# Kernel tuning notes

Hardware: AMD Instinct MI355X
Metric: run time of the kernel (lower is better)

Reference implementation:

```python
import jax, jax.numpy as jnp
import numpy as np

DIM = 1024
HEADS = 8
DIM_HEAD = 64
HIDDEN = HEADS * DIM_HEAD  # 512
SCALE = DIM_HEAD ** -0.5
BATCH = 16384
EPS = 1e-12  # F.normalize eps


def setup_inputs() -> dict:
    key = jax.random.key(0)
    k0, k1, k2 = jax.random.split(key, 3)
    x = jax.random.normal(k0, (BATCH, DIM), dtype=jnp.float32)
    w_qkv = jax.random.normal(k1, (3 * HIDDEN, DIM), dtype=jnp.float32) * 0.02
    w_out = jax.random.normal(k2, (DIM, HIDDEN), dtype=jnp.float32) * 0.02
    b_out = jnp.zeros((DIM,), dtype=jnp.float32)
    g = jnp.ones((1, DIM), dtype=jnp.float32)
    return {"x": x, "w_qkv": w_qkv, "w_out": w_out, "b_out": b_out, "g": g}


def reference(x, w_qkv, w_out, b_out, g):
    b = x.shape[0]
    # Conv1d(kernel=1, no bias) on n=1 sequence == matmul with (3*hidden, dim) weight
    qkv = x @ w_qkv.T  # (b, 3*hidden)
    q, k, v = jnp.split(qkv, 3, axis=1)  # each (b, hidden)
    # rearrange 'b (h c) n -> b h c n' with n=1 -> (b, h, c)
    q = q.reshape(b, HEADS, DIM_HEAD)
    k = k.reshape(b, HEADS, DIM_HEAD)
    v = v.reshape(b, HEADS, DIM_HEAD)
    # q.softmax(dim=-2) is over the c axis
    q = jax.nn.softmax(q, axis=-1) * SCALE
    # k.softmax(dim=-1) is over the n axis of size 1 -> all ones (kept faithful)
    k = jax.nn.softmax(k[..., None], axis=-1)[..., 0]
    # context = einsum('bhdn,bhen->bhde', k, v); out = einsum('bhde,bhdn->bhen', context, q)
    # with n=1 this collapses to out_e = (sum_d k_d q_d) * v_e; fused to avoid (b,h,d,e)
    s = jnp.einsum('bhd,bhd->bh', k, q)  # (b, h)
    out = s[..., None] * v  # (b, h, e)
    out = out.reshape(b, HIDDEN)  # 'b h c n -> b (h c) n', squeeze(-1)
    # Linear(hidden, dim)
    out = out @ w_out.T + b_out  # (b, dim)
    # RMSNorm_MLP: F.normalize(x, dim=1) * g * sqrt(dim)
    norm = jnp.linalg.norm(out, axis=1, keepdims=True)
    out = out / jnp.maximum(norm, EPS) * g * jnp.sqrt(jnp.float32(DIM))
    return out
```

## Files before the change

### kernel.cpp

```cpp
#include <hip/hip_runtime.h>
#include <hip/hip_bf16.h>


typedef __attribute__((ext_vector_type(8))) short bf16x8;
typedef __attribute__((ext_vector_type(4))) float f32x4;

struct alignas(16) bfvec8 { __hip_bfloat16 h[8]; };

__device__ __forceinline__ bfvec8 pack8(float4 a, float4 b) {
    bfvec8 o;
    o.h[0] = __float2bfloat16(a.x); o.h[1] = __float2bfloat16(a.y);
    o.h[2] = __float2bfloat16(a.z); o.h[3] = __float2bfloat16(a.w);
    o.h[4] = __float2bfloat16(b.x); o.h[5] = __float2bfloat16(b.y);
    o.h[6] = __float2bfloat16(b.z); o.h[7] = __float2bfloat16(b.w);
    return o;
}

__global__ __launch_bounds__(256)
void weff_fused(const float* __restrict__ Wo, const float* __restrict__ Wv,
                __hip_bfloat16* __restrict__ Weff) {
    __shared__ __align__(16) __hip_bfloat16 As[64 * 32];
    __shared__ __align__(16) __hip_bfloat16 Bs[64 * 32];
    __shared__ __align__(16) float Bf[32 * 65];

    const int tid  = threadIdx.x;
    const int lane = tid & 63;
    const int wave = tid >> 6;
    const int wm   = wave >> 1;
    const int wn   = wave & 1;
    const int quad = lane >> 4;
    const int tr   = lane & 15;
    const int m0   = blockIdx.y * 64;
    const int n0   = blockIdx.x * 64;

    f32x4 acc[2][2];
#pragma unroll
    for (int i = 0; i < 2; ++i)
#pragma unroll
        for (int j = 0; j < 2; ++j)
            acc[i][j] = (f32x4){0.f, 0.f, 0.f, 0.f};

    for (int kt = 0; kt < 512; kt += 32) {
        {
            int r = tid >> 2, c = tid & 3;
            int s = (r >> 1) & 3;
            int kg = (c ^ s) << 3;
            const float* sp = Wo + (size_t)(m0 + r) * 512 + kt + kg;
            float4 a = *(const float4*)sp, b = *(const float4*)(sp + 4);
            *(bfvec8*)(As + r * 32 + (c << 3)) = pack8(a, b);
        }
        {
            int kr = tid >> 3, c8 = (tid & 7) << 3;
            const float* sp = Wv + (size_t)(kt + kr) * 1024 + n0 + c8;
            float4 a = *(const float4*)sp, b = *(const float4*)(sp + 4);
            *(float4*)(Bf + kr * 65 + c8)     = a;
            *(float4*)(Bf + kr * 65 + c8 + 4) = b;
        }
        __syncthreads();
        {
            int n = tid >> 2, cc = tid & 3, k8 = cc << 3;
            float4 a, b;
            a.x = Bf[(k8 + 0) * 65 + n]; a.y = Bf[(k8 + 1) * 65 + n];
            a.z = Bf[(k8 + 2) * 65 + n]; a.w = Bf[(k8 + 3) * 65 + n];
            b.x = Bf[(k8 + 4) * 65 + n]; b.y = Bf[(k8 + 5) * 65 + n];
            b.z = Bf[(k8 + 6) * 65 + n]; b.w = Bf[(k8 + 7) * 65 + n];
            int cs = cc ^ ((n >> 1) & 3);
            *(bfvec8*)(Bs + n * 32 + cs * 8) = pack8(a, b);
        }
        __syncthreads();

        bf16x8 af[2], bf[2];
#pragma unroll
        for (int mi = 0; mi < 2; ++mi) {
            int r = wm * 32 + mi * 16 + tr;
            int c = quad ^ ((r >> 1) & 3);
            af[mi] = *(const bf16x8*)(As + r * 32 + c * 8);
        }
#pragma unroll
        for (int ni = 0; ni < 2; ++ni) {
            int r = wn * 32 + ni * 16 + tr;
            int c = quad ^ ((r >> 1) & 3);
            bf[ni] = *(const bf16x8*)(Bs + r * 32 + c * 8);
        }
#pragma unroll
        for (int mi = 0; mi < 2; ++mi)
#pragma unroll
            for (int ni = 0; ni < 2; ++ni)
                acc[mi][ni] = __builtin_amdgcn_mfma_f32_16x16x32_bf16(
                    af[mi], bf[ni], acc[mi][ni], 0, 0, 0);
        __syncthreads();
    }

#pragma unroll
    for (int mi = 0; mi < 2; ++mi)
#pragma unroll
        for (int ni = 0; ni < 2; ++ni) {
            const int col = n0 + wn * 32 + ni * 16 + tr;
#pragma unroll
            for (int r = 0; r < 4; ++r) {
                const int row = m0 + wm * 32 + mi * 16 + quad * 4 + r;
                Weff[(size_t)row * 1024 + col] =
                    __float2bfloat16(acc[mi][ni][r] * 0.125f);
            }
        }
}

__global__ __launch_bounds__(256)
void main_gemm(const float* __restrict__ X,
               const __hip_bfloat16* __restrict__ Bt,
               const float* __restrict__ bias,
               __hip_bfloat16* __restrict__ Y) {
    __shared__ __align__(16) __hip_bfloat16 As[128 * 64];
    __shared__ __align__(16) __hip_bfloat16 Bs[128 * 64];

    const int tid  = threadIdx.x;
    const int lane = tid & 63;
    const int wave = tid >> 6;
    const int wm   = wave >> 1;
    const int wn   = wave & 1;
    const int quad = lane >> 4;
    const int tr   = lane & 15;

    const int b   = blockIdx.x;
    const int xcd = b & 7;
    const int t   = b >> 3;
    const int nt  = t & 7;
    const int mt  = (t >> 3) * 8 + xcd;
    const int m0  = mt * 128;
    const int n0  = nt * 128;

    int rr[4], kgg[4];
    size_t abase[4];
#pragma unroll
    for (int i = 0; i < 4; ++i) {
        int L = i * 256 + tid;
        rr[i]  = L >> 3;
        int c  = L & 7;
        kgg[i] = (c ^ (rr[i] & 7)) << 3;
        abase[i] = (size_t)(m0 + rr[i]) * 1024 + kgg[i];
    }

    f32x4 acc[4][4];
#pragma unroll
    for (int i = 0; i < 4; ++i)
#pragma unroll
        for (int j = 0; j < 4; ++j)
            acc[i][j] = (f32x4){0.f, 0.f, 0.f, 0.f};

    float4 pa[4], pb[4];
#pragma unroll
    for (int i = 0; i < 4; ++i) {
        const float* s = X + abase[i];
        pa[i] = *(const float4*)s;
        pb[i] = *(const float4*)(s + 4);
    }

    for (int kt = 0; kt < 1024; kt += 64) {
#pragma unroll
        for (int i = 0; i < 4; ++i) {
            int L = i * 256 + tid;
            const __hip_bfloat16* gb = Bt + (size_t)(n0 + rr[i]) * 1024 + kt + kgg[i];
            __builtin_amdgcn_global_load_lds(
                (const __attribute__((address_space(1))) void*)gb,
                (__attribute__((address_space(3))) void*)(Bs + (size_t)L * 8), 16, 0, 0);
        }
#pragma unroll
        for (int i = 0; i < 4; ++i) {
            int L = i * 256 + tid;
            *(bfvec8*)(As + (size_t)L * 8) = pack8(pa[i], pb[i]);
        }
        __syncthreads();

        if (kt + 64 < 1024) {
#pragma unroll
            for (int i = 0; i < 4; ++i) {
                const float* s = X + abase[i] + kt + 64;
                pa[i] = *(const float4*)s;
                pb[i] = *(const float4*)(s + 4);
            }
        }

#pragma unroll
        for (int ko = 0; ko < 2; ++ko) {
            bf16x8 af[4], bf[4];
#pragma unroll
            for (int mi = 0; mi < 4; ++mi) {
                int r = wm * 64 + mi * 16 + tr;
                int c = (ko * 4 + quad) ^ (r & 7);
                af[mi] = *(const bf16x8*)(As + (r * 8 + c) * 8);
            }
#pragma unroll
            for (int ni = 0; ni < 4; ++ni) {
                int r = wn * 64 + ni * 16 + tr;
                int c = (ko * 4 + quad) ^ (r & 7);
                bf[ni] = *(const bf16x8*)(Bs + (r * 8 + c) * 8);
            }
#pragma unroll
            for (int mi = 0; mi < 4; ++mi)
#pragma unroll
                for (int ni = 0; ni < 4; ++ni)
                    acc[mi][ni] = __builtin_amdgcn_mfma_f32_16x16x32_bf16(
                        af[mi], bf[ni], acc[mi][ni], 0, 0, 0);
        }
        __syncthreads();
    }

#pragma unroll
    for (int mi = 0; mi < 4; ++mi)
#pragma unroll
        for (int ni = 0; ni < 4; ++ni) {
            const int col = n0 + wn * 64 + ni * 16 + tr;
            const float bv = bias[col];
#pragma unroll
            for (int r = 0; r < 4; ++r) {
                const int row = m0 + wm * 64 + mi * 16 + quad * 4 + r;
                Y[(size_t)row * 1024 + col] = __float2bfloat16(acc[mi][ni][r] + bv);
            }
        }
}

__global__ __launch_bounds__(256)
void rmsnorm2(const __hip_bfloat16* __restrict__ y, const float* __restrict__ g,
              float* __restrict__ out) {
    const int wave = threadIdx.x >> 6;
    const int sub  = wave >> 1;
    const int t    = threadIdx.x & 127;
    const int row  = blockIdx.x * 2 + sub;
    const size_t base = (size_t)row * 1024 + t * 8;

    union { uint4 u; ushort s[8]; } U;
    U.u = *(const uint4*)(y + base);
    float v[8];
#pragma unroll
    for (int j = 0; j < 8; ++j)
        v[j] = __bfloat162float(*(const __hip_bfloat16*)&U.s[j]);

    float ss = 0.f;
#pragma unroll
    for (int j = 0; j < 8; ++j) ss += v[j] * v[j];
#pragma unroll
    for (int off = 32; off > 0; off >>= 1)
        ss += __shfl_down(ss, off, 64);

    __shared__ float wsum[4];
    if ((threadIdx.x & 63) == 0) wsum[wave] = ss;
    __syncthreads();
    const float total = wsum[sub * 2] + wsum[sub * 2 + 1];
    const float sc = 32.0f / fmaxf(sqrtf(total), 1e-12f);

    const float4 g0 = *(const float4*)(g + t * 8);
    const float4 g1 = *(const float4*)(g + t * 8 + 4);
    float4 o0, o1;
    o0.x = v[0] * sc * g0.x; o0.y = v[1] * sc * g0.y;
    o0.z = v[2] * sc * g0.z; o0.w = v[3] * sc * g0.w;
    o1.x = v[4] * sc * g1.x; o1.y = v[5] * sc * g1.y;
    o1.z = v[6] * sc * g1.z; o1.w = v[7] * sc * g1.w;
    *(float4*)(out + base)     = o0;
    *(float4*)(out + base + 4) = o1;
}

extern "C" void kernel_launch(void* const* d_in, const int* in_sizes, int n_in,
                              void* d_out, int out_size, void* d_ws, size_t ws_size,
                              hipStream_t stream) {
    const float* x     = (const float*)d_in[0];
    const float* w_qkv = (const float*)d_in[1];
    const float* w_out = (const float*)d_in[2];
    const float* b_out = (const float*)d_in[3];
    const float* g     = (const float*)d_in[4];

    const int B = 16384, D = 1024, H = 512;
    const float* wv = w_qkv + (size_t)2 * H * D;

    char* ws = (char*)d_ws;
    size_t off = 0;
    __hip_bfloat16* weff_bf = (__hip_bfloat16*)(ws + off); off += (size_t)D * D * 2;
    __hip_bfloat16* y_bf    = (__hip_bfloat16*)(ws + off); off += (size_t)B * D * 2;

    weff_fused<<<dim3(D / 64, D / 64), 256, 0, stream>>>(w_out, wv, weff_bf);
    main_gemm<<<1024, 256, 0, stream>>>(x, weff_bf, b_out, y_bf);
    rmsnorm2<<<B / 2, 256, 0, stream>>>(y_bf, g, (float*)d_out);
}
```

Before: 190.5 us.

## Double-buffer LDS tiles in main GEMM to overlap loads with MFMA

Doubles the shared-memory buffers for A and B in the main GEMM and restructures the k-loop so the next tile's global-to-LDS B load and the A bf16 conversion/store happen while MFMAs run on the current tile. This cuts the loop from two barriers per iteration to one, with manual s_waitcnt and sched_barrier control. It doubles LDS use to 64KB per block, which may lower occupancy, and relies on hand-counted vmcnt values being correct.

```diff
diff --git a/kernel.cpp b/kernel.cpp
--- a/kernel.cpp
+++ b/kernel.cpp
@@ -105,13 +105,42 @@
         }
 }
 
+
+__device__ __forceinline__ void mfma_tile(const __hip_bfloat16* Ac,
+                                          const __hip_bfloat16* Bc,
+                                          f32x4 (&acc)[4][4],
+                                          int wm, int wn, int quad, int tr) {
+#pragma unroll
+    for (int ko = 0; ko < 2; ++ko) {
+        bf16x8 af[4], bf[4];
+#pragma unroll
+        for (int mi = 0; mi < 4; ++mi) {
+            int r = wm * 64 + mi * 16 + tr;
+            int c = (ko * 4 + quad) ^ (r & 7);
+            af[mi] = *(const bf16x8*)(Ac + (r * 8 + c) * 8);
+        }
+#pragma unroll
+        for (int ni = 0; ni < 4; ++ni) {
+            int r = wn * 64 + ni * 16 + tr;
+            int c = (ko * 4 + quad) ^ (r & 7);
+            bf[ni] = *(const bf16x8*)(Bc + (r * 8 + c) * 8);
+        }
+#pragma unroll
+        for (int mi = 0; mi < 4; ++mi)
+#pragma unroll
+            for (int ni = 0; ni < 4; ++ni)
+                acc[mi][ni] = __builtin_amdgcn_mfma_f32_16x16x32_bf16(
+                    af[mi], bf[ni], acc[mi][ni], 0, 0, 0);
+    }
+}
+
 __global__ __launch_bounds__(256)
 void main_gemm(const float* __restrict__ X,
                const __hip_bfloat16* __restrict__ Bt,
                const float* __restrict__ bias,
                __hip_bfloat16* __restrict__ Y) {
-    __shared__ __align__(16) __hip_bfloat16 As[128 * 64];
-    __shared__ __align__(16) __hip_bfloat16 Bs[128 * 64];
+    __shared__ __align__(16) __hip_bfloat16 As[2 * 128 * 64];
+    __shared__ __align__(16) __hip_bfloat16 Bs[2 * 128 * 64];
 
     const int tid  = threadIdx.x;
     const int lane = tid & 63;
@@ -123,21 +152,24 @@
 
     const int b   = blockIdx.x;
     const int xcd = b & 7;
-    const int t   = b >> 3;
-    const int nt  = t & 7;
-    const int mt  = (t >> 3) * 8 + xcd;
-    const int m0  = mt * 128;
-    const int n0  = nt * 128;
-
-    int rr[4], kgg[4];
+    const int tb  = b >> 3;
+    const int ntl = tb & 7;
+    const int mtl = (tb >> 3) * 8 + xcd;
+    const int m0  = mtl * 128;
+    const int n0  = ntl * 128;
+
+    int rr[4], kgg[4], ldst[4];
     size_t abase[4];
+    const __hip_bfloat16* bbase[4];
 #pragma unroll
     for (int i = 0; i < 4; ++i) {
         int L = i * 256 + tid;
-        rr[i]  = L >> 3;
-        int c  = L & 7;
-        kgg[i] = (c ^ (rr[i] & 7)) << 3;
+        rr[i]   = L >> 3;
+        int c   = L & 7;
+        kgg[i]  = (c ^ (rr[i] & 7)) << 3;
+        ldst[i] = L * 8;
         abase[i] = (size_t)(m0 + rr[i]) * 1024 + kgg[i];
+        bbase[i] = Bt + (size_t)(n0 + rr[i]) * 1024 + kgg[i];
     }
 
     f32x4 acc[4][4];
@@ -146,6 +178,11 @@
 #pragma unroll
         for (int j = 0; j < 4; ++j)
             acc[i][j] = (f32x4){0.f, 0.f, 0.f, 0.f};
+
+    __hip_bfloat16* Ac = As;
+    __hip_bfloat16* An = As + 128 * 64;
+    __hip_bfloat16* Bc = Bs;
+    __hip_bfloat16* Bn = Bs + 128 * 64;
 
     float4 pa[4], pb[4];
 #pragma unroll
@@ -154,56 +191,56 @@
         pa[i] = *(const float4*)s;
         pb[i] = *(const float4*)(s + 4);
     }
-
-    for (int kt = 0; kt < 1024; kt += 64) {
-#pragma unroll
-        for (int i = 0; i < 4; ++i) {
-            int L = i * 256 + tid;
-            const __hip_bfloat16* gb = Bt + (size_t)(n0 + rr[i]) * 1024 + kt + kgg[i];
+#pragma unroll
+    for (int i = 0; i < 4; ++i)
+        __builtin_amdgcn_global_load_lds(
+            (const __attribute__((address_space(1))) void*)(bbase[i]),
+            (__attribute__((address_space(3))) void*)(Bc + ldst[i]), 16, 0, 0);
+#pragma unroll
+    for (int i = 0; i < 4; ++i)
+        *(bfvec8*)(Ac + ldst[i]) = pack8(pa[i], pb[i]);
+    __syncthreads();
+#pragma unroll
+    for (int i = 0; i < 4; ++i) {
+        const float* s = X + abase[i] + 64;
+        pa[i] = *(const float4*)s;
+        pb[i] = *(const float4*)(s + 4);
+    }
+
+    for (int t = 0; t < 15; ++t) {
+        const int koff = (t + 1) * 64;
+
+#pragma unroll
+        for (int i = 0; i < 4; ++i)
             __builtin_amdgcn_global_load_lds(
-                (const __attribute__((address_space(1))) void*)gb,
-                (__attribute__((address_space(3))) void*)(Bs + (size_t)L * 8), 16, 0, 0);
-        }
-#pragma unroll
-        for (int i = 0; i < 4; ++i) {
-            int L = i * 256 + tid;
-            *(bfvec8*)(As + (size_t)L * 8) = pack8(pa[i], pb[i]);
-        }
-        __syncthreads();
-
-        if (kt + 64 < 1024) {
+                (const __attribute__((address_space(1))) void*)(bbase[i] + koff),
+                (__attribute__((address_space(3))) void*)(Bn + ldst[i]), 16, 0, 0);
+        __builtin_amdgcn_sched_barrier(0);
+
+        mfma_tile(Ac, Bc, acc, wm, wn, quad, tr);
+
+#pragma unroll
+        for (int i = 0; i < 4; ++i)
+            *(bfvec8*)(An + ldst[i]) = pack8(pa[i], pb[i]);
+
+        if (t < 14) {
 #pragma unroll
             for (int i = 0; i < 4; ++i) {
-                const float* s = X + abase[i] + kt + 64;
+                const float* s = X + abase[i] + koff + 64;
                 pa[i] = *(const float4*)s;
                 pb[i] = *(const float4*)(s + 4);
             }
-        }
-
-#pragma unroll
-        for (int ko = 0; ko < 2; ++ko) {
-            bf16x8 af[4], bf[4];
-#pragma unroll
-            for (int mi = 0; mi < 4; ++mi) {
-                int r = wm * 64 + mi * 16 + tr;
-                int c = (ko * 4 + quad) ^ (r & 7);
-                af[mi] = *(const bf16x8*)(As + (r * 8 + c) * 8);
-            }
-#pragma unroll
-            for (int ni = 0; ni < 4; ++ni) {
-                int r = wn * 64 + ni * 16 + tr;
-                int c = (ko * 4 + quad) ^ (r & 7);
-                bf[ni] = *(const bf16x8*)(Bs + (r * 8 + c) * 8);
-            }
-#pragma unroll
-            for (int mi = 0; mi < 4; ++mi)
-#pragma unroll
-                for (int ni = 0; ni < 4; ++ni)
-                    acc[mi][ni] = __builtin_amdgcn_mfma_f32_16x16x32_bf16(
-                        af[mi], bf[ni], acc[mi][ni], 0, 0, 0);
-        }
-        __syncthreads();
-    }
+            asm volatile("s_waitcnt vmcnt(8) lgkmcnt(0)" ::: "memory");
+        } else {
+            asm volatile("s_waitcnt vmcnt(0) lgkmcnt(0)" ::: "memory");
+        }
+        __builtin_amdgcn_sched_barrier(0);
+        __builtin_amdgcn_s_barrier();
+
+        __hip_bfloat16* tA = Ac; Ac = An; An = tA;
+        __hip_bfloat16* tB = Bc; Bc = Bn; Bn = tB;
+    }
+    mfma_tile(Ac, Bc, acc, wm, wn, quad, tr);
 
 #pragma unroll
     for (int mi = 0; mi < 4; ++mi)
```

Result: no change. 193.4 us (+1.5%).

## Pre-convert X to bf16 in prep kernel and rewrite main GEMM pipeline

Applied to the files above, without the earlier changes.

Adds a grid-stride pass to the Weff prep kernel that converts X to bf16 in a new workspace buffer. The main GEMM can then stream both operands straight into LDS with global_load_lds. The GEMM becomes 256x256 tiles with 512 threads, double-buffered LDS, staged async loads interleaved with MFMA phases, explicit waitcnt/barrier scheduling and setprio. This aims to hide load latency and raise MFMA utilization, at the cost of an extra 32MB bf16 write and read of X and a fragile hand-tuned sync schedule.

```diff
diff --git a/kernel.cpp b/kernel.cpp
--- a/kernel.cpp
+++ b/kernel.cpp
@@ -17,21 +17,34 @@
 }
 
 __global__ __launch_bounds__(256)
-void weff_fused(const float* __restrict__ Wo, const float* __restrict__ Wv,
-                __hip_bfloat16* __restrict__ Weff) {
+void prep(const float* __restrict__ Wo, const float* __restrict__ Wv,
+          __hip_bfloat16* __restrict__ Weff,
+          const float* __restrict__ X, __hip_bfloat16* __restrict__ Xbf) {
     __shared__ __align__(16) __hip_bfloat16 As[64 * 32];
     __shared__ __align__(16) __hip_bfloat16 Bs[64 * 32];
     __shared__ __align__(16) float Bf[32 * 65];
 
-    const int tid  = threadIdx.x;
+    const int tid = threadIdx.x;
+
+    if (blockIdx.x >= 256) {
+        const size_t nv = (size_t)16384 * 1024 / 8;
+        const size_t stride = (size_t)2048 * 256;
+        for (size_t i = (size_t)(blockIdx.x - 256) * 256 + tid; i < nv; i += stride) {
+            const float4 a = *(const float4*)(X + i * 8);
+            const float4 b = *(const float4*)(X + i * 8 + 4);
+            *(bfvec8*)(Xbf + i * 8) = pack8(a, b);
+        }
+        return;
+    }
+
     const int lane = tid & 63;
     const int wave = tid >> 6;
     const int wm   = wave >> 1;
     const int wn   = wave & 1;
     const int quad = lane >> 4;
     const int tr   = lane & 15;
-    const int m0   = blockIdx.y * 64;
-    const int n0   = blockIdx.x * 64;
+    const int m0   = (blockIdx.x >> 4) * 64;
+    const int n0   = (blockIdx.x & 15) * 64;
 
     f32x4 acc[2][2];
 #pragma unroll
@@ -69,7 +82,7 @@
         }
         __syncthreads();
 
-        bf16x8 af[2], bf[2];
+        bf16x8 af[2], bfr[2];
 #pragma unroll
         for (int mi = 0; mi < 2; ++mi) {
             int r = wm * 32 + mi * 16 + tr;
@@ -80,14 +93,14 @@
         for (int ni = 0; ni < 2; ++ni) {
             int r = wn * 32 + ni * 16 + tr;
             int c = quad ^ ((r >> 1) & 3);
-            bf[ni] = *(const bf16x8*)(Bs + r * 32 + c * 8);
+            bfr[ni] = *(const bf16x8*)(Bs + r * 32 + c * 8);
         }
 #pragma unroll
         for (int mi = 0; mi < 2; ++mi)
 #pragma unroll
             for (int ni = 0; ni < 2; ++ni)
                 acc[mi][ni] = __builtin_amdgcn_mfma_f32_16x16x32_bf16(
-                    af[mi], bf[ni], acc[mi][ni], 0, 0, 0);
+                    af[mi], bfr[ni], acc[mi][ni], 0, 0, 0);
         __syncthreads();
     }
 
@@ -105,118 +118,142 @@
         }
 }
 
-__global__ __launch_bounds__(256)
-void main_gemm(const float* __restrict__ X,
+
+#define GLL(gp, lp) __builtin_amdgcn_global_load_lds( \
+    (const __attribute__((address_space(1))) void*)(gp), \
+    (__attribute__((address_space(3))) void*)(lp), 16, 0, 0)
+
+#define STAGE_A(BUF, H, U) do { \
+    GLL(Xbf + Ab0 + (size_t)(H) * 131072 + (size_t)(U) * 64, \
+        sm + (BUF) * 32768 + (H) * 8192 + ldsA);             \
+    GLL(Xbf + Ab1 + (size_t)(H) * 131072 + (size_t)(U) * 64, \
+        sm + (BUF) * 32768 + (H) * 8192 + 4096 + ldsA);      \
+} while (0)
+
+#define STAGE_B(BUF, H, U) do { \
+    GLL(Bt + Bb0 + (size_t)(H) * 131072 + (size_t)(U) * 64,  \
+        sm + (BUF) * 32768 + 16384 + (H) * 8192 + ldsA);     \
+    GLL(Bt + Bb1 + (size_t)(H) * 131072 + (size_t)(U) * 64,  \
+        sm + (BUF) * 32768 + 16384 + (H) * 8192 + 4096 + ldsA); \
+} while (0)
+
+__global__ __launch_bounds__(512, 2)
+void main_gemm(const __hip_bfloat16* __restrict__ Xbf,
                const __hip_bfloat16* __restrict__ Bt,
                const float* __restrict__ bias,
                __hip_bfloat16* __restrict__ Y) {
-    __shared__ __align__(16) __hip_bfloat16 As[128 * 64];
-    __shared__ __align__(16) __hip_bfloat16 Bs[128 * 64];
+    __shared__ __align__(16) __hip_bfloat16 sm[2 * 32768];
 
     const int tid  = threadIdx.x;
     const int lane = tid & 63;
-    const int wave = tid >> 6;
-    const int wm   = wave >> 1;
-    const int wn   = wave & 1;
+    const int wc   = tid >> 6;
     const int quad = lane >> 4;
     const int tr   = lane & 15;
-
-    const int b   = blockIdx.x;
-    const int xcd = b & 7;
-    const int t   = b >> 3;
-    const int nt  = t & 7;
-    const int mt  = (t >> 3) * 8 + xcd;
-    const int m0  = mt * 128;
-    const int n0  = nt * 128;
-
-    int rr[4], kgg[4];
-    size_t abase[4];
-#pragma unroll
-    for (int i = 0; i < 4; ++i) {
-        int L = i * 256 + tid;
-        rr[i]  = L >> 3;
-        int c  = L & 7;
-        kgg[i] = (c ^ (rr[i] & 7)) << 3;
-        abase[i] = (size_t)(m0 + rr[i]) * 1024 + kgg[i];
+    const int rlow = tr & 7;
+
+    const int xcd  = blockIdx.x & 7;
+    const int orig = xcd * 32 + (blockIdx.x >> 3);
+    const int m0   = (orig >> 2) * 256;
+    const int n0   = (orig & 3) * 256;
+
+    const int r0 = tid >> 3,            c0 = tid & 7;
+    const int r1 = (tid + 512) >> 3,    c1 = tid & 7;
+    const size_t Ab0 = (size_t)(m0 + r0) * 1024 + ((c0 ^ (r0 & 7)) << 3);
+    const size_t Ab1 = (size_t)(m0 + r1) * 1024 + ((c1 ^ (r1 & 7)) << 3);
+    const size_t Bb0 = (size_t)(n0 + r0) * 1024 + ((c0 ^ (r0 & 7)) << 3);
+    const size_t Bb1 = (size_t)(n0 + r1) * 1024 + ((c1 ^ (r1 & 7)) << 3);
+    const int ldsA = tid * 8;
+
+    int ac[2];
+#pragma unroll
+    for (int ko = 0; ko < 2; ++ko) ac[ko] = ((ko * 4 + quad) ^ rlow) * 8;
+    const int rdA = tr * 64;
+    const int rdB = wc * 2048 + tr * 64;
+
+    f32x4 acc[16][2];
+#pragma unroll
+    for (int f = 0; f < 16; ++f)
+#pragma unroll
+        for (int ni = 0; ni < 2; ++ni)
+            acc[f][ni] = (f32x4){0.f, 0.f, 0.f, 0.f};
+
+    STAGE_B(0, 0, 0); STAGE_B(0, 1, 0); STAGE_A(0, 0, 0); STAGE_A(0, 1, 0);
+    STAGE_B(1, 0, 1); STAGE_B(1, 1, 1); STAGE_A(1, 0, 1);
+    asm volatile("s_waitcnt vmcnt(6)" ::: "memory");
+    __builtin_amdgcn_s_barrier();
+
+    bf16x8 bfr[2][2];
+
+    for (int it = 0; it < 8; ++it) {
+#pragma unroll
+        for (int rb = 0; rb < 2; ++rb) {
+            const int u = it * 2 + rb;
+#pragma unroll
+            for (int p = 0; p < 4; ++p) {
+                bf16x8 af[4][2];
+#pragma unroll
+                for (int mi = 0; mi < 4; ++mi)
+#pragma unroll
+                    for (int ko = 0; ko < 2; ++ko)
+                        af[mi][ko] = *(const bf16x8*)(
+                            sm + rb * 32768 + p * 4096 + mi * 1024 + rdA + ac[ko]);
+                if (p == 0) {
+#pragma unroll
+                    for (int ni = 0; ni < 2; ++ni)
+#pragma unroll
+                        for (int ko = 0; ko < 2; ++ko)
+                            bfr[ni][ko] = *(const bf16x8*)(
+                                sm + rb * 32768 + 16384 + rdB + ni * 1024 + ac[ko]);
+                }
+
+                if (p == 0)      { if (u + 1 < 16) STAGE_A(rb ^ 1, 1, u + 1); }
+                else if (p == 1) { if (u + 2 < 16) STAGE_B(rb, 0, u + 2); }
+                else if (p == 2) { if (u + 2 < 16) STAGE_B(rb, 1, u + 2); }
+                else             { if (u + 2 < 16) STAGE_A(rb, 0, u + 2); }
+
+                if (p == 0) asm volatile("s_waitcnt lgkmcnt(8)" ::: "memory");
+                __builtin_amdgcn_s_barrier();
+                asm volatile("s_waitcnt lgkmcnt(0)" ::: "memory");
+                __builtin_amdgcn_sched_barrier(0);
+
+                __builtin_amdgcn_s_setprio(1);
+#pragma unroll
+                for (int mi = 0; mi < 4; ++mi)
+#pragma unroll
+                    for (int ni = 0; ni < 2; ++ni)
+#pragma unroll
+                        for (int ko = 0; ko < 2; ++ko)
+                            acc[p * 4 + mi][ni] = __builtin_amdgcn_mfma_f32_16x16x32_bf16(
+                                af[mi][ko], bfr[ni][ko], acc[p * 4 + mi][ni], 0, 0, 0);
+                __builtin_amdgcn_s_setprio(0);
+
+                if (p == 3) {
+                    if (u <= 13)      asm volatile("s_waitcnt vmcnt(6)" ::: "memory");
+                    else if (u == 14) asm volatile("s_waitcnt vmcnt(0)" ::: "memory");
+                    if (u < 15) __builtin_amdgcn_s_barrier();
+                } else {
+                    __builtin_amdgcn_s_barrier();
+                }
+            }
+        }
     }
 
-    f32x4 acc[4][4];
-#pragma unroll
-    for (int i = 0; i < 4; ++i)
-#pragma unroll
-        for (int j = 0; j < 4; ++j)
-            acc[i][j] = (f32x4){0.f, 0.f, 0.f, 0.f};
-
-    float4 pa[4], pb[4];
-#pragma unroll
-    for (int i = 0; i < 4; ++i) {
-        const float* s = X + abase[i];
-        pa[i] = *(const float4*)s;
-        pb[i] = *(const float4*)(s + 4);
+    float bv[2]; int col[2];
+#pragma unroll
+    for (int ni = 0; ni < 2; ++ni) {
+        col[ni] = n0 + wc * 32 + ni * 16 + tr;
+        bv[ni]  = bias[col[ni]];
     }
-
-    for (int kt = 0; kt < 1024; kt += 64) {
-#pragma unroll
-        for (int i = 0; i < 4; ++i) {
-            int L = i * 256 + tid;
-            const __hip_bfloat16* gb = Bt + (size_t)(n0 + rr[i]) * 1024 + kt + kgg[i];
-            __builtin_amdgcn_global_load_lds(
-                (const __attribute__((address_space(1))) void*)gb,
-                (__attribute__((address_space(3))) void*)(Bs + (size_t)L * 8), 16, 0, 0);
-        }
-#pragma unroll
-        for (int i = 0; i < 4; ++i) {
-            int L = i * 256 + tid;
-            *(bfvec8*)(As + (size_t)L * 8) = pack8(pa[i], pb[i]);
-        }
-        __syncthreads();
-
-        if (kt + 64 < 1024) {
-#pragma unroll
-            for (int i = 0; i < 4; ++i) {
-                const float* s = X + abase[i] + kt + 64;
-                pa[i] = *(const float4*)s;
-                pb[i] = *(const float4*)(s + 4);
+#pragma unroll
+    for (int f = 0; f < 16; ++f)
+#pragma unroll
+        for (int ni = 0; ni < 2; ++ni)
+#pragma unroll
+            for (int rr = 0; rr < 4; ++rr) {
+                const int row = m0 + f * 16 + quad * 4 + rr;
+                Y[(size_t)row * 1024 + col[ni]] =
+                    __float2bfloat16(acc[f][ni][rr] + bv[ni]);
             }
-        }
-
-#pragma unroll
-        for (int ko = 0; ko < 2; ++ko) {
-            bf16x8 af[4], bf[4];
-#pragma unroll
-            for (int mi = 0; mi < 4; ++mi) {
-                int r = wm * 64 + mi * 16 + tr;
-                int c = (ko * 4 + quad) ^ (r & 7);
-                af[mi] = *(const bf16x8*)(As + (r * 8 + c) * 8);
-            }
-#pragma unroll
-            for (int ni = 0; ni < 4; ++ni) {
-                int r = wn * 64 + ni * 16 + tr;
-                int c = (ko * 4 + quad) ^ (r & 7);
-                bf[ni] = *(const bf16x8*)(Bs + (r * 8 + c) * 8);
-            }
-#pragma unroll
-            for (int mi = 0; mi < 4; ++mi)
-#pragma unroll
-                for (int ni = 0; ni < 4; ++ni)
-                    acc[mi][ni] = __builtin_amdgcn_mfma_f32_16x16x32_bf16(
-                        af[mi], bf[ni], acc[mi][ni], 0, 0, 0);
-        }
-        __syncthreads();
-    }
-
-#pragma unroll
-    for (int mi = 0; mi < 4; ++mi)
-#pragma unroll
-        for (int ni = 0; ni < 4; ++ni) {
-            const int col = n0 + wn * 64 + ni * 16 + tr;
-            const float bv = bias[col];
-#pragma unroll
-            for (int r = 0; r < 4; ++r) {
-                const int row = m0 + wm * 64 + mi * 16 + quad * 4 + r;
-                Y[(size_t)row * 1024 + col] = __float2bfloat16(acc[mi][ni][r] + bv);
-            }
-        }
 }
 
 __global__ __launch_bounds__(256)
@@ -275,8 +312,9 @@
     size_t off = 0;
     __hip_bfloat16* weff_bf = (__hip_bfloat16*)(ws + off); off += (size_t)D * D * 2;
     __hip_bfloat16* y_bf    = (__hip_bfloat16*)(ws + off); off += (size_t)B * D * 2;
-
-    weff_fused<<<dim3(D / 64, D / 64), 256, 0, stream>>>(w_out, wv, weff_bf);
-    main_gemm<<<1024, 256, 0, stream>>>(x, weff_bf, b_out, y_bf);
+    __hip_bfloat16* x_bf    = (__hip_bfloat16*)(ws + off); off += (size_t)B * D * 2;
+
+    prep<<<256 + 2048, 256, 0, stream>>>(w_out, wv, weff_bf, x, x_bf);
+    main_gemm<<<256, 512, 0, stream>>>(x_bf, weff_bf, b_out, y_bf);
     rmsnorm2<<<B / 2, 256, 0, stream>>>(y_bf, g, (float*)d_out);
 }
```

Measured after the change: 178.4 us. -6.3%, faster.

## Fuse main GEMM with RMSNorm using full-row 64x1024 block tiles

Applied to the files above, without the earlier changes.

Replaces the separate main GEMM and RMSNorm kernels with one kernel. Each 512-thread block computes a full 64-row by 1024-column output tile, so the row norm can be reduced in-block and fp32 output written directly. This removes the bf16 intermediate Y write and re-read and one kernel launch. The main loop double-buffers 32-wide K tiles through LDS using direct global-to-LDS loads, with explicit waitcnt and priority hints. In exchange it uses a large LDS footprint and a single block per CU across 256 blocks, which lowers occupancy and latency hiding.

```diff
diff --git a/kernel.cpp b/kernel.cpp
--- a/kernel.cpp
+++ b/kernel.cpp
@@ -6,6 +6,7 @@
 typedef __attribute__((ext_vector_type(4))) float f32x4;
 
 struct alignas(16) bfvec8 { __hip_bfloat16 h[8]; };
+struct alignas(8)  bfvec4 { __hip_bfloat16 h[4]; };
 
 __device__ __forceinline__ bfvec8 pack8(float4 a, float4 b) {
     bfvec8 o;
@@ -16,9 +17,16 @@
     return o;
 }
 
+__device__ __forceinline__ bfvec4 pack4(float4 a) {
+    bfvec4 o;
+    o.h[0] = __float2bfloat16(a.x); o.h[1] = __float2bfloat16(a.y);
+    o.h[2] = __float2bfloat16(a.z); o.h[3] = __float2bfloat16(a.w);
+    return o;
+}
+
 __global__ __launch_bounds__(256)
-void weff_fused(const float* __restrict__ Wo, const float* __restrict__ Wv,
-                __hip_bfloat16* __restrict__ Weff) {
+void weff_only(const float* __restrict__ Wo, const float* __restrict__ Wv,
+               __hip_bfloat16* __restrict__ Weff) {
     __shared__ __align__(16) __hip_bfloat16 As[64 * 32];
     __shared__ __align__(16) __hip_bfloat16 Bs[64 * 32];
     __shared__ __align__(16) float Bf[32 * 65];
@@ -30,8 +38,8 @@
     const int wn   = wave & 1;
     const int quad = lane >> 4;
     const int tr   = lane & 15;
-    const int m0   = blockIdx.y * 64;
-    const int n0   = blockIdx.x * 64;
+    const int m0   = (blockIdx.x >> 4) * 64;
+    const int n0   = (blockIdx.x & 15) * 64;
 
     f32x4 acc[2][2];
 #pragma unroll
@@ -69,7 +77,7 @@
         }
         __syncthreads();
 
-        bf16x8 af[2], bf[2];
+        bf16x8 af[2], bfr[2];
 #pragma unroll
         for (int mi = 0; mi < 2; ++mi) {
             int r = wm * 32 + mi * 16 + tr;
@@ -80,14 +88,14 @@
         for (int ni = 0; ni < 2; ++ni) {
             int r = wn * 32 + ni * 16 + tr;
             int c = quad ^ ((r >> 1) & 3);
-            bf[ni] = *(const bf16x8*)(Bs + r * 32 + c * 8);
+            bfr[ni] = *(const bf16x8*)(Bs + r * 32 + c * 8);
         }
 #pragma unroll
         for (int mi = 0; mi < 2; ++mi)
 #pragma unroll
             for (int ni = 0; ni < 2; ++ni)
                 acc[mi][ni] = __builtin_amdgcn_mfma_f32_16x16x32_bf16(
-                    af[mi], bf[ni], acc[mi][ni], 0, 0, 0);
+                    af[mi], bfr[ni], acc[mi][ni], 0, 0, 0);
         __syncthreads();
     }
 
@@ -105,158 +113,155 @@
         }
 }
 
-__global__ __launch_bounds__(256)
-void main_gemm(const float* __restrict__ X,
-               const __hip_bfloat16* __restrict__ Bt,
-               const float* __restrict__ bias,
-               __hip_bfloat16* __restrict__ Y) {
-    __shared__ __align__(16) __hip_bfloat16 As[128 * 64];
-    __shared__ __align__(16) __hip_bfloat16 Bs[128 * 64];
+
+#define GLL(gp, lp) __builtin_amdgcn_global_load_lds( \
+    (const __attribute__((address_space(1))) void*)(gp), \
+    (__attribute__((address_space(3))) void*)(lp), 16, 0, 0)
+
+__global__ __launch_bounds__(512, 2)
+void main_fused(const float* __restrict__ X,
+                const __hip_bfloat16* __restrict__ W,
+                const float* __restrict__ bias,
+                const float* __restrict__ g,
+                float* __restrict__ out) {
+    __shared__ __align__(16) __hip_bfloat16 sm[69632];
+    __shared__ float wpart[8][64];
+    __shared__ float scrow[64];
 
     const int tid  = threadIdx.x;
     const int lane = tid & 63;
-    const int wave = tid >> 6;
-    const int wm   = wave >> 1;
-    const int wn   = wave & 1;
+    const int wc   = tid >> 6;
     const int quad = lane >> 4;
     const int tr   = lane & 15;
 
-    const int b   = blockIdx.x;
-    const int xcd = b & 7;
-    const int t   = b >> 3;
-    const int nt  = t & 7;
-    const int mt  = (t >> 3) * 8 + xcd;
-    const int m0  = mt * 128;
-    const int n0  = nt * 128;
-
-    int rr[4], kgg[4];
-    size_t abase[4];
-#pragma unroll
-    for (int i = 0; i < 4; ++i) {
-        int L = i * 256 + tid;
-        rr[i]  = L >> 3;
-        int c  = L & 7;
-        kgg[i] = (c ^ (rr[i] & 7)) << 3;
-        abase[i] = (size_t)(m0 + rr[i]) * 1024 + kgg[i];
-    }
-
-    f32x4 acc[4][4];
-#pragma unroll
-    for (int i = 0; i < 4; ++i)
-#pragma unroll
-        for (int j = 0; j < 4; ++j)
-            acc[i][j] = (f32x4){0.f, 0.f, 0.f, 0.f};
-
-    float4 pa[4], pb[4];
-#pragma unroll
-    for (int i = 0; i < 4; ++i) {
-        const float* s = X + abase[i];
-        pa[i] = *(const float4*)s;
-        pb[i] = *(const float4*)(s + 4);
-    }
-
-    for (int kt = 0; kt < 1024; kt += 64) {
-#pragma unroll
-        for (int i = 0; i < 4; ++i) {
-            int L = i * 256 + tid;
-            const __hip_bfloat16* gb = Bt + (size_t)(n0 + rr[i]) * 1024 + kt + kgg[i];
-            __builtin_amdgcn_global_load_lds(
-                (const __attribute__((address_space(1))) void*)gb,
-                (__attribute__((address_space(3))) void*)(Bs + (size_t)L * 8), 16, 0, 0);
-        }
-#pragma unroll
-        for (int i = 0; i < 4; ++i) {
-            int L = i * 256 + tid;
-            *(bfvec8*)(As + (size_t)L * 8) = pack8(pa[i], pb[i]);
-        }
-        __syncthreads();
-
-        if (kt + 64 < 1024) {
-#pragma unroll
-            for (int i = 0; i < 4; ++i) {
-                const float* s = X + abase[i] + kt + 64;
-                pa[i] = *(const float4*)s;
-                pb[i] = *(const float4*)(s + 4);
+    const int m0 = blockIdx.x * 64;
+
+    const int ra = tid >> 3, q = tid & 7;
+    const int aq = (((q >> 1) ^ (ra & 3)) << 3) + (q & 1) * 4;
+    const float* Ag = X + (size_t)(m0 + ra) * 1024 + aq;
+    const int AdsW = tid * 4;
+
+    const int brow = tid >> 2;
+    const int kswz = (((tid & 3) ^ (brow & 3)) << 3);
+
+    const int ac = ((quad ^ (tr & 3)) << 3);
+
+    f32x4 acc[4][8];
+#pragma unroll
+    for (int mi = 0; mi < 4; ++mi)
+#pragma unroll
+        for (int ni = 0; ni < 8; ++ni)
+            acc[mi][ni] = (f32x4){0.f, 0.f, 0.f, 0.f};
+
+    {
+#pragma unroll
+        for (int i = 0; i < 4; ++i)
+            GLL(W + (size_t)(i * 128 + brow) * 1024 + kswz,
+                sm + 4096 + (i * 512 + tid) * 8);
+        float4 pav = *(const float4*)Ag;
+#pragma unroll
+        for (int i = 4; i < 8; ++i)
+            GLL(W + (size_t)(i * 128 + brow) * 1024 + kswz,
+                sm + 4096 + (i * 512 + tid) * 8);
+        asm volatile("s_waitcnt vmcnt(4)" ::: "memory");
+        *(bfvec4*)(sm + AdsW) = pack4(pav);
+        asm volatile("s_waitcnt vmcnt(0) lgkmcnt(0)" ::: "memory");
+        __builtin_amdgcn_s_barrier();
+    }
+
+#define TILE(U, RB) do { \
+    const int u_ = (U); \
+    float4 pav; \
+    if (u_ < 31) { \
+        const int kt_ = (u_ + 1) * 32; \
+        _Pragma("unroll") \
+        for (int i = 0; i < 4; ++i) \
+            GLL(W + (size_t)(i * 128 + brow) * 1024 + kt_ + kswz, \
+                sm + 4096 + ((RB) ^ 1) * 32768 + (i * 512 + tid) * 8); \
+        pav = *(const float4*)(Ag + kt_); \
+        _Pragma("unroll") \
+        for (int i = 4; i < 8; ++i) \
+            GLL(W + (size_t)(i * 128 + brow) * 1024 + kt_ + kswz, \
+                sm + 4096 + ((RB) ^ 1) * 32768 + (i * 512 + tid) * 8); \
+    } \
+    bf16x8 af[4], bfr[8]; \
+    _Pragma("unroll") \
+    for (int mi = 0; mi < 4; ++mi) \
+        af[mi] = *(const bf16x8*)(sm + (RB) * 2048 + (mi * 16 + tr) * 32 + ac); \
+    _Pragma("unroll") \
+    for (int ni = 0; ni < 8; ++ni) \
+        bfr[ni] = *(const bf16x8*)(sm + 4096 + (RB) * 32768 + \
+                                   (wc * 128 + ni * 16 + tr) * 32 + ac); \
+    asm volatile("s_waitcnt lgkmcnt(0)" ::: "memory"); \
+    __builtin_amdgcn_sched_barrier(0); \
+    __builtin_amdgcn_s_setprio(1); \
+    _Pragma("unroll") \
+    for (int mi = 0; mi < 4; ++mi) \
+        _Pragma("unroll") \
+        for (int ni = 0; ni < 8; ++ni) \
+            acc[mi][ni] = __builtin_amdgcn_mfma_f32_16x16x32_bf16( \
+                af[mi], bfr[ni], acc[mi][ni], 0, 0, 0); \
+    __builtin_amdgcn_s_setprio(0); \
+    if (u_ < 31) { \
+        asm volatile("s_waitcnt vmcnt(4)" ::: "memory"); \
+        *(bfvec4*)(sm + ((RB) ^ 1) * 2048 + AdsW) = pack4(pav); \
+    } \
+    asm volatile("s_waitcnt vmcnt(0) lgkmcnt(0)" ::: "memory"); \
+    __builtin_amdgcn_s_barrier(); \
+} while (0)
+
+    for (int it = 0; it < 16; ++it) {
+        TILE(it * 2,     0);
+        TILE(it * 2 + 1, 1);
+    }
+#undef TILE
+
+    float bvv[8], gvv[8];
+    int coln[8];
+#pragma unroll
+    for (int ni = 0; ni < 8; ++ni) {
+        coln[ni] = wc * 128 + ni * 16 + tr;
+        bvv[ni] = bias[coln[ni]];
+        gvv[ni] = g[coln[ni]];
+    }
+
+#pragma unroll
+    for (int mi = 0; mi < 4; ++mi)
+#pragma unroll
+        for (int rr = 0; rr < 4; ++rr) {
+            float p = 0.f;
+#pragma unroll
+            for (int ni = 0; ni < 8; ++ni) {
+                const float t = acc[mi][ni][rr] + bvv[ni];
+                acc[mi][ni][rr] = t;
+                p += t * t;
             }
-        }
-
-#pragma unroll
-        for (int ko = 0; ko < 2; ++ko) {
-            bf16x8 af[4], bf[4];
-#pragma unroll
-            for (int mi = 0; mi < 4; ++mi) {
-                int r = wm * 64 + mi * 16 + tr;
-                int c = (ko * 4 + quad) ^ (r & 7);
-                af[mi] = *(const bf16x8*)(As + (r * 8 + c) * 8);
-            }
-#pragma unroll
-            for (int ni = 0; ni < 4; ++ni) {
-                int r = wn * 64 + ni * 16 + tr;
-                int c = (ko * 4 + quad) ^ (r & 7);
-                bf[ni] = *(const bf16x8*)(Bs + (r * 8 + c) * 8);
-            }
-#pragma unroll
-            for (int mi = 0; mi < 4; ++mi)
-#pragma unroll
-                for (int ni = 0; ni < 4; ++ni)
-                    acc[mi][ni] = __builtin_amdgcn_mfma_f32_16x16x32_bf16(
-                        af[mi], bf[ni], acc[mi][ni], 0, 0, 0);
-        }
-        __syncthreads();
-    }
+#pragma unroll
+            for (int msk = 1; msk < 16; msk <<= 1)
+                p += __shfl_xor(p, msk, 64);
+            if (tr == 0) wpart[wc][mi * 16 + quad * 4 + rr] = p;
+        }
+    __syncthreads();
+
+    if (tid < 64) {
+        float s = 0.f;
+#pragma unroll
+        for (int w = 0; w < 8; ++w) s += wpart[w][tid];
+        scrow[tid] = 32.0f / fmaxf(sqrtf(s), 1e-12f);
+    }
+    __syncthreads();
 
 #pragma unroll
     for (int mi = 0; mi < 4; ++mi)
 #pragma unroll
-        for (int ni = 0; ni < 4; ++ni) {
-            const int col = n0 + wn * 64 + ni * 16 + tr;
-            const float bv = bias[col];
-#pragma unroll
-            for (int r = 0; r < 4; ++r) {
-                const int row = m0 + wm * 64 + mi * 16 + quad * 4 + r;
-                Y[(size_t)row * 1024 + col] = __float2bfloat16(acc[mi][ni][r] + bv);
-            }
-        }
-}
-
-__global__ __launch_bounds__(256)
-void rmsnorm2(const __hip_bfloat16* __restrict__ y, const float* __restrict__ g,
-              float* __restrict__ out) {
-    const int wave = threadIdx.x >> 6;
-    const int sub  = wave >> 1;
-    const int t    = threadIdx.x & 127;
-    const int row  = blockIdx.x * 2 + sub;
-    const size_t base = (size_t)row * 1024 + t * 8;
-
-    union { uint4 u; ushort s[8]; } U;
-    U.u = *(const uint4*)(y + base);
-    float v[8];
-#pragma unroll
-    for (int j = 0; j < 8; ++j)
-        v[j] = __bfloat162float(*(const __hip_bfloat16*)&U.s[j]);
-
-    float ss = 0.f;
-#pragma unroll
-    for (int j = 0; j < 8; ++j) ss += v[j] * v[j];
-#pragma unroll
-    for (int off = 32; off > 0; off >>= 1)
-        ss += __shfl_down(ss, off, 64);
-
-    __shared__ float wsum[4];
-    if ((threadIdx.x & 63) == 0) wsum[wave] = ss;
-    __syncthreads();
-    const float total = wsum[sub * 2] + wsum[sub * 2 + 1];
-    const float sc = 32.0f / fmaxf(sqrtf(total), 1e-12f);
-
-    const float4 g0 = *(const float4*)(g + t * 8);
-    const float4 g1 = *(const float4*)(g + t * 8 + 4);
-    float4 o0, o1;
-    o0.x = v[0] * sc * g0.x; o0.y = v[1] * sc * g0.y;
-    o0.z = v[2] * sc * g0.z; o0.w = v[3] * sc * g0.w;
-    o1.x = v[4] * sc * g1.x; o1.y = v[5] * sc * g1.y;
-    o1.z = v[6] * sc * g1.z; o1.w = v[7] * sc * g1.w;
-    *(float4*)(out + base)     = o0;
-    *(float4*)(out + base + 4) = o1;
+        for (int rr = 0; rr < 4; ++rr) {
+            const int r16 = mi * 16 + quad * 4 + rr;
+            const float sc = scrow[r16];
+#pragma unroll
+            for (int ni = 0; ni < 8; ++ni)
+                out[(size_t)(m0 + r16) * 1024 + coln[ni]] =
+                    acc[mi][ni][rr] * sc * gvv[ni];
+        }
 }
 
 extern "C" void kernel_launch(void* const* d_in, const int* in_sizes, int n_in,
@@ -268,15 +273,11 @@
     const float* b_out = (const float*)d_in[3];
     const float* g     = (const float*)d_in[4];
 
-    const int B = 16384, D = 1024, H = 512;
+    const int D = 1024, H = 512;
     const float* wv = w_qkv + (size_t)2 * H * D;
 
-    char* ws = (char*)d_ws;
-    size_t off = 0;
-    __hip_bfloat16* weff_bf = (__hip_bfloat16*)(ws + off); off += (size_t)D * D * 2;
-    __hip_bfloat16* y_bf    = (__hip_bfloat16*)(ws + off); off += (size_t)B * D * 2;
-
-    weff_fused<<<dim3(D / 64, D / 64), 256, 0, stream>>>(w_out, wv, weff_bf);
-    main_gemm<<<1024, 256, 0, stream>>>(x, weff_bf, b_out, y_bf);
-    rmsnorm2<<<B / 2, 256, 0, stream>>>(y_bf, g, (float*)d_out);
-}
+    __hip_bfloat16* weff_bf = (__hip_bfloat16*)d_ws;
+
+    weff_only<<<256, 256, 0, stream>>>(w_out, wv, weff_bf);
+    main_fused<<<256, 512, 0, stream>>>(x, weff_bf, b_out, g, (float*)d_out);
+}
```

Result: faster. 179.6 us (-5.7%).
